# Performance work log

Hardware: AMD Instinct MI355X
Metric: run time of the kernel (lower is better)

Reference implementation:

```python
import jax, jax.numpy as jnp
import numpy as np

MSA_DIM = 256
N_HEADS = 8
HEAD_DIM = 32
INNER = N_HEADS * HEAD_DIM


def setup_inputs() -> dict:
    key = jax.random.key(0)
    ks = jax.random.split(key, 8)
    B, S, L, D = 1, 256, 256, MSA_DIM
    scale = 1.0 / np.sqrt(D)
    msa = jax.random.normal(ks[0], (B, S, L, D), dtype=jnp.float32)
    return {
        "msa": msa,
        "ln_gamma": jnp.ones((D,), jnp.float32),
        "ln_beta": jnp.zeros((D,), jnp.float32),
        "W_q": jax.random.normal(ks[1], (D, INNER), jnp.float32) * scale,
        "W_k": jax.random.normal(ks[2], (D, INNER), jnp.float32) * scale,
        "W_v": jax.random.normal(ks[3], (D, INNER), jnp.float32) * scale,
        "W_g": jax.random.normal(ks[4], (D, INNER), jnp.float32) * scale,
        "b_g": jnp.zeros((INNER,), jnp.float32),
        "W_o": jax.random.normal(ks[5], (INNER, D), jnp.float32) * (1.0 / np.sqrt(INNER)),
        "b_o": jnp.zeros((D,), jnp.float32),
    }


def _layernorm(x, gamma, beta, eps=1e-5):
    mu = jnp.mean(x, axis=-1, keepdims=True)
    var = jnp.mean(jnp.square(x - mu), axis=-1, keepdims=True)
    return (x - mu) * jax.lax.rsqrt(var + eps) * gamma + beta


def reference(msa, ln_gamma, ln_beta, W_q, W_k, W_v, W_g, b_g, W_o, b_o):
    B, S, L, D = msa.shape
    factor = 1.0 / np.sqrt(HEAD_DIM)
    x = _layernorm(msa, ln_gamma, ln_beta)  # [B,S,L,D]
    def proj(W):
        return (x @ W).reshape(B, S, L, N_HEADS, HEAD_DIM)
    Q = proj(W_q) * factor
    K = proj(W_k)
    V = proj(W_v)
    # column attention: attend over the num_seqs axis (i,j) per column c
    attn = jnp.einsum('bicnh,bjcnh->bncij', Q, K)  # [B,H,L,S,S]
    attn = jax.nn.softmax(attn, axis=-1)
    gate = jax.nn.sigmoid(x @ W_g + b_g).reshape(B, S, L, N_HEADS, HEAD_DIM)
    out = jnp.einsum('bncij,bjcnh->bicnh', attn, V) * gate
    out = out.reshape(B, S, L, INNER)
    return out @ W_o + b_o
```

## Files before the change

### kernel.cpp

```cpp
#include <hip/hip_runtime.h>
#include <hip/hip_bf16.h>


typedef __attribute__((ext_vector_type(8))) short bf16x8;
typedef __attribute__((ext_vector_type(4))) float fx4;

__device__ __forceinline__ fx4 mfma(bf16x8 a, bf16x8 b, fx4 c) {
  return __builtin_amdgcn_mfma_f32_16x16x32_bf16(a, b, c, 0, 0, 0);
}
__device__ __forceinline__ fx4 fx4zero() {
  fx4 z;
  z[0] = 0.f; z[1] = 0.f; z[2] = 0.f; z[3] = 0.f;
  return z;
}
__device__ __forceinline__ unsigned short f2bf(float f) {
  unsigned u = __float_as_uint(f);
  u += 0x7fffu + ((u >> 16) & 1u);
  return (unsigned short)(u >> 16);
}
__device__ __forceinline__ float bf2f(unsigned short h) {
  return __uint_as_float(((unsigned)h) << 16);
}
__device__ __forceinline__ unsigned pk2(float a, float b) {
  __hip_bfloat162 t = __float22bfloat162_rn(make_float2(a, b));
  return *reinterpret_cast<unsigned*>(&t);
}
__device__ __forceinline__ float asf(unsigned u) { return __uint_as_float(u); }
__device__ __forceinline__ unsigned shflu(unsigned v, int src) {
  return (unsigned)__shfl((int)v, src, 64);
}

__global__ __launch_bounds__(256) void k_wprep(
    const float* __restrict__ Wq, const float* __restrict__ Wk,
    const float* __restrict__ Wv, const float* __restrict__ Wg,
    const float* __restrict__ Wo, const float* __restrict__ gamma,
    const float* __restrict__ beta,
    unsigned short* __restrict__ wch, unsigned short* __restrict__ wcl,
    unsigned short* __restrict__ woh, unsigned short* __restrict__ wol,
    float* __restrict__ uarr, float* __restrict__ tarr) {
  __shared__ float red[8];
  const int n = blockIdx.x, k = threadIdx.x;
  const int lane = k & 63, wid = k >> 6;
  if (n < 1024) {
    int h = n >> 7, nl = n & 127, m = nl >> 5, col = h * 32 + (nl & 31);
    const float* W = (m == 0) ? Wq : (m == 1) ? Wk : (m == 2) ? Wv : Wg;
    float v = W[k * 256 + col];
    if (m == 0) v *= 0.17677669529663687f;
    float w2 = gamma[k] * v;
    unsigned short hi = f2bf(w2);
    wch[(size_t)n * 256 + k] = hi;
    wcl[(size_t)n * 256 + k] = f2bf(w2 - bf2f(hi));
    float u = w2, t = beta[k] * v;
#pragma unroll
    for (int d = 1; d < 64; d <<= 1) {
      u += __shfl_xor(u, d);
      t += __shfl_xor(t, d);
    }
    if (lane == 0) { red[wid] = u; red[4 + wid] = t; }
    __syncthreads();
    if (k == 0) {
      uarr[n] = red[0] + red[1] + red[2] + red[3];
      tarr[n] = red[4] + red[5] + red[6] + red[7];
    }
  } else {
    int nn = n - 1024;
    float v = Wo[k * 256 + nn];
    unsigned short hi = f2bf(v);
    woh[(size_t)nn * 256 + k] = hi;
    wol[(size_t)nn * 256 + k] = f2bf(v - bf2f(hi));
  }
}

__global__ __launch_bounds__(256) void k_pre(
    const float* __restrict__ msa,
    unsigned short* __restrict__ xh, unsigned short* __restrict__ xl,
    float2* __restrict__ stats) {
  int rid = blockIdx.x * 4 + (threadIdx.x >> 6);
  int lane = threadIdx.x & 63;
  float4 v = ((const float4*)(msa + (size_t)rid * 256))[lane];
  float s = v.x + v.y + v.z + v.w;
  float ss = v.x * v.x + v.y * v.y + v.z * v.z + v.w * v.w;
#pragma unroll
  for (int d = 1; d < 64; d <<= 1) {
    s += __shfl_xor(s, d);
    ss += __shfl_xor(ss, d);
  }
  unsigned h01 = pk2(v.x, v.y);
  unsigned h23 = pk2(v.z, v.w);
  float l0 = v.x - asf(h01 << 16);
  float l1 = v.y - asf(h01 & 0xffff0000u);
  float l2 = v.z - asf(h23 << 16);
  float l3 = v.w - asf(h23 & 0xffff0000u);
  uint2 hh, ll;
  hh.x = h01; hh.y = h23;
  ll.x = pk2(l0, l1); ll.y = pk2(l2, l3);
  int srow = rid >> 8, l = rid & 255;
  size_t o = ((size_t)(l * 256 + srow)) * 256 + lane * 4;
  *(uint2*)(xh + o) = hh;
  *(uint2*)(xl + o) = ll;
  if (lane == 0) {
    float mu = s * (1.f / 256.f);
    float rstd = rsqrtf(ss * (1.f / 256.f) - mu * mu + 1e-5f);
    stats[l * 256 + srow] = make_float2(mu, rstd);
  }
}

#define N_WAH 0
#define N_WAL 10240
#define N_WBH 20480
#define N_WBL 30720
#define N_KH 0
#define N_KL 20480
#define N_VTH 40960
#define N_VTL 57856

__global__ __launch_bounds__(512, 4) void k_fused_pre(
    const float* __restrict__ bg,
    const unsigned short* __restrict__ wch, const unsigned short* __restrict__ wcl,
    const float* __restrict__ uarr, const float* __restrict__ tarr,
    const unsigned short* __restrict__ xh, const unsigned short* __restrict__ xl,
    const float2* __restrict__ stats,
    float* __restrict__ O) {
  __shared__ __align__(16) char smem[74752];
  const int tid = threadIdx.x, lane = tid & 63, wid = tid >> 6;
  const int l15 = lane & 15, q4 = lane >> 4;
  const int l = (blockIdx.x & 7) * 32 + (blockIdx.x >> 6);
  const int h = (blockIdx.x >> 3) & 7;
  const size_t xbase = ((size_t)l * 256) * 256;

  fx4 acc[2][8];
#pragma unroll
  for (int i = 0; i < 2; ++i)
#pragma unroll
    for (int j = 0; j < 8; ++j) acc[i][j] = fx4zero();

  const int snl = tid >> 2, skc = tid & 3;
  const size_t wgi = (size_t)(h * 128 + snl) * 256 + skc * 8;
  const int soff = snl * 80 + skc * 16;

  {
    *(int4*)&smem[N_WAH + soff] = *(const int4*)(wch + wgi);
    *(int4*)&smem[N_WAL + soff] = *(const int4*)(wcl + wgi);
  }
  __syncthreads();

  for (int c = 0; c < 8; ++c) {
    int4 wnh, wnl;
    if (c < 7) {
      wnh = *(const int4*)(wch + wgi + (c + 1) * 32);
      wnl = *(const int4*)(wcl + wgi + (c + 1) * 32);
    }
    bf16x8 xa[2], xb[2];
#pragma unroll
    for (int fi = 0; fi < 2; ++fi) {
      size_t ga = xbase + (size_t)(wid * 32 + fi * 16 + l15) * 256 + c * 32 + q4 * 8;
      xa[fi] = *(const bf16x8*)(xh + ga);
      xb[fi] = *(const bf16x8*)(xl + ga);
    }
    const int wbh = (c & 1) ? N_WBH : N_WAH;
#pragma unroll
    for (int nh = 0; nh < 2; ++nh) {
#pragma unroll
      for (int fj = 0; fj < 4; ++fj) {
        int off = (nh * 64 + fj * 16 + l15) * 80 + q4 * 16;
        bf16x8 bh = *(const bf16x8*)&smem[wbh + off];
        bf16x8 bl = *(const bf16x8*)&smem[wbh + 10240 + off];
#pragma unroll
        for (int fi = 0; fi < 2; ++fi) {
          fx4 a = acc[fi][nh * 4 + fj];
          a = mfma(xa[fi], bh, a);
          a = mfma(xb[fi], bh, a);
          a = mfma(xa[fi], bl, a);
          acc[fi][nh * 4 + fj] = a;
        }
      }
    }
    if (c < 7) {
      const int wb2 = (c & 1) ? N_WAH : N_WBH;
      *(int4*)&smem[wb2 + soff] = wnh;
      *(int4*)&smem[wb2 + 10240 + soff] = wnl;
      __syncthreads();
    }
  }
  __syncthreads();

  float uv[8], tv[8];
#pragma unroll
  for (int fj = 0; fj < 8; ++fj) {
    int ng = h * 128 + fj * 16 + l15;
    uv[fj] = uarr[ng];
    tv[fj] = tarr[ng];
  }
  float bgv[2];
#pragma unroll
  for (int fd = 0; fd < 2; ++fd) bgv[fd] = bg[h * 32 + fd * 16 + l15];
  const int cb = l15 * 2;
  const int qbh = wid * 2560, qbl = 20480 + wid * 2560;

#pragma unroll
  for (int fi = 0; fi < 2; ++fi)
#pragma unroll
    for (int r = 0; r < 4; ++r) {
      int s = wid * 32 + fi * 16 + q4 * 4 + r;
      int il = fi * 16 + q4 * 4 + r;
      float2 st = stats[l * 256 + s];
      float y0 = st.y * (acc[fi][0][r] - st.x * uv[0]) + tv[0];
      float y1 = st.y * (acc[fi][1][r] - st.x * uv[1]) + tv[1];
      unsigned hp = pk2(y0, y1);
      unsigned lp = pk2(y0 - asf(hp << 16), y1 - asf(hp & 0xffff0000u));
      *(unsigned short*)&smem[qbh + il * 80 + cb] = (unsigned short)hp;
      *(unsigned short*)&smem[qbh + il * 80 + 32 + cb] = (unsigned short)(hp >> 16);
      *(unsigned short*)&smem[qbl + il * 80 + cb] = (unsigned short)lp;
      *(unsigned short*)&smem[qbl + il * 80 + 32 + cb] = (unsigned short)(lp >> 16);
    }
  asm volatile("s_waitcnt lgkmcnt(0)" ::: "memory");
  __builtin_amdgcn_sched_barrier(0);
  bf16x8 qh[2], ql[2];
#pragma unroll
  for (int fi = 0; fi < 2; ++fi) {
    int off = (fi * 16 + l15) * 80 + q4 * 16;
    qh[fi] = *(const bf16x8*)&smem[qbh + off];
    ql[fi] = *(const bf16x8*)&smem[qbl + off];
  }

  float gt[2][2][4];
#pragma unroll
  for (int fi = 0; fi < 2; ++fi) {
    float y4[4], y5[4];
#pragma unroll
    for (int r = 0; r < 4; ++r) {
      int s = wid * 32 + fi * 16 + q4 * 4 + r;
      float2 st = stats[l * 256 + s];
      {
        float y0 = st.y * (acc[fi][2][r] - st.x * uv[2]) + tv[2];
        float y1 = st.y * (acc[fi][3][r] - st.x * uv[3]) + tv[3];
        unsigned hp = pk2(y0, y1);
        unsigned lp = pk2(y0 - asf(hp << 16), y1 - asf(hp & 0xffff0000u));
        *(unsigned short*)&smem[N_KH + s * 80 + cb] = (unsigned short)hp;
        *(unsigned short*)&smem[N_KH + s * 80 + 32 + cb] = (unsigned short)(hp >> 16);
        *(unsigned short*)&smem[N_KL + s * 80 + cb] = (unsigned short)lp;
        *(unsigned short*)&smem[N_KL + s * 80 + 32 + cb] = (unsigned short)(lp >> 16);
      }
      y4[r] = st.y * (acc[fi][4][r] - st.x * uv[4]) + tv[4];
      y5[r] = st.y * (acc[fi][5][r] - st.x * uv[5]) + tv[5];
      float y6 = st.y * (acc[fi][6][r] - st.x * uv[6]) + tv[6];
      float y7 = st.y * (acc[fi][7][r] - st.x * uv[7]) + tv[7];
      gt[fi][0][r] = 1.f / (1.f + __expf(-(y6 + bgv[0])));
      gt[fi][1][r] = 1.f / (1.f + __expf(-(y7 + bgv[1])));
    }
    int s0 = wid * 32 + fi * 16 + q4 * 4;
    uint2 vh4, vl4, vh5, vl5;
    vh4.x = pk2(y4[0], y4[1]); vh4.y = pk2(y4[2], y4[3]);
    vl4.x = pk2(y4[0] - asf(vh4.x << 16), y4[1] - asf(vh4.x & 0xffff0000u));
    vl4.y = pk2(y4[2] - asf(vh4.y << 16), y4[3] - asf(vh4.y & 0xffff0000u));
    vh5.x = pk2(y5[0], y5[1]); vh5.y = pk2(y5[2], y5[3]);
    vl5.x = pk2(y5[0] - asf(vh5.x << 16), y5[1] - asf(vh5.x & 0xffff0000u));
    vl5.y = pk2(y5[2] - asf(vh5.y << 16), y5[3] - asf(vh5.y & 0xffff0000u));
    *(uint2*)&smem[N_VTH + l15 * 528 + s0 * 2] = vh4;
    *(uint2*)&smem[N_VTH + (16 + l15) * 528 + s0 * 2] = vh5;
    *(uint2*)&smem[N_VTL + l15 * 528 + s0 * 2] = vl4;
    *(uint2*)&smem[N_VTL + (16 + l15) * 528 + s0 * 2] = vl5;
  }
  __syncthreads();

  fx4 oacc[2][2];
  float lsum[2] = {0.f, 0.f};
  oacc[0][0] = fx4zero(); oacc[0][1] = fx4zero();
  oacc[1][0] = fx4zero(); oacc[1][1] = fx4zero();

  const int srcA = ((q4 & 1) << 5) + l15;
  const int srcB = srcA + 16;
  const bool fhi = (q4 >> 1) != 0;

  for (int jc = 0; jc < 8; ++jc) {
    const int j0 = jc * 32;
    bf16x8 kh[2], kl[2];
#pragma unroll
    for (int fj = 0; fj < 2; ++fj) {
      int off = (j0 + fj * 16 + l15) * 80 + q4 * 16;
      kh[fj] = *(const bf16x8*)&smem[N_KH + off];
      kl[fj] = *(const bf16x8*)&smem[N_KL + off];
    }
    bf16x8 vbh[2], vbl[2];
#pragma unroll
    for (int fd = 0; fd < 2; ++fd) {
      int off = (fd * 16 + l15) * 528 + j0 * 2 + q4 * 16;
      vbh[fd] = *(const bf16x8*)&smem[N_VTH + off];
      vbl[fd] = *(const bf16x8*)&smem[N_VTL + off];
    }
    fx4 sT[2][2];
    __builtin_amdgcn_s_setprio(1);
#pragma unroll
    for (int fi = 0; fi < 2; ++fi)
#pragma unroll
      for (int fj = 0; fj < 2; ++fj) {
        fx4 a = mfma(kh[fj], qh[fi], fx4zero());
        a = mfma(kh[fj], ql[fi], a);
        a = mfma(kl[fj], qh[fi], a);
        sT[fi][fj] = a;
      }
    __builtin_amdgcn_s_setprio(0);
#pragma unroll
    for (int fi = 0; fi < 2; ++fi) {
      float p0[4], p1[4];
#pragma unroll
      for (int r = 0; r < 4; ++r) {
        p0[r] = __expf(sT[fi][0][r]);
        p1[r] = __expf(sT[fi][1][r]);
      }
      lsum[fi] += ((p0[0] + p0[1]) + (p0[2] + p0[3])) +
                  ((p1[0] + p1[1]) + (p1[2] + p1[3]));
      unsigned A0 = pk2(p0[0], p0[1]), A1 = pk2(p0[2], p0[3]);
      unsigned B0 = pk2(p1[0], p1[1]), B1 = pk2(p1[2], p1[3]);
      unsigned a0A = shflu(A0, srcA), b0A = shflu(B0, srcA);
      unsigned a1A = shflu(A1, srcA), b1A = shflu(B1, srcA);
      unsigned a0B = shflu(A0, srcB), b0B = shflu(B0, srcB);
      unsigned a1B = shflu(A1, srcB), b1B = shflu(B1, srcB);
      int4 wh;
      wh.x = (int)(fhi ? b0A : a0A);
      wh.y = (int)(fhi ? b1A : a1A);
      wh.z = (int)(fhi ? b0B : a0B);
      wh.w = (int)(fhi ? b1B : a1B);
      bf16x8 pah = *reinterpret_cast<bf16x8*>(&wh);
      __builtin_amdgcn_s_setprio(1);
#pragma unroll
      for (int fd = 0; fd < 2; ++fd) {
        fx4 a = oacc[fi][fd];
        a = mfma(pah, vbh[fd], a);
        a = mfma(pah, vbl[fd], a);
        oacc[fi][fd] = a;
      }
      __builtin_amdgcn_s_setprio(0);
    }
  }

  float lsr[2][4];
#pragma unroll
  for (int fi = 0; fi < 2; ++fi) {
    float t = lsum[fi];
    t += __shfl_xor(t, 16);
    t += __shfl_xor(t, 32);
#pragma unroll
    for (int r = 0; r < 4; ++r)
      lsr[fi][r] = __shfl(t, q4 * 4 + r, 64);
  }

#pragma unroll
  for (int fi = 0; fi < 2; ++fi)
#pragma unroll
    for (int r = 0; r < 4; ++r) {
      float inv = 1.f / lsr[fi][r];
      int s = wid * 32 + fi * 16 + q4 * 4 + r;
#pragma unroll
      for (int fd = 0; fd < 2; ++fd) {
        int hd = fd * 16 + l15;
        O[((size_t)(s * 256 + l)) * 256 + h * 32 + hd] =
            oacc[fi][fd][r] * inv * gt[fi][fd][r];
      }
    }
}

#define S_XH 0
#define S_XL 20480
#define S_WH 40960
#define S_WL 51200
#define S_KPH 0
#define S_KPL 20480
#define S_VTH 40960
#define S_VTL 57856
#define S_QPH 74752
#define S_QPL 95232
#define S_ST 115712

__global__ __launch_bounds__(512, 2) void k_fused_fb(
    const float* __restrict__ msa, const float* __restrict__ bg,
    const unsigned short* __restrict__ wch, const unsigned short* __restrict__ wcl,
    const float* __restrict__ uarr, const float* __restrict__ tarr,
    float* __restrict__ O) {
  __shared__ __align__(16) char smem[117760];
  const int tid = threadIdx.x, lane = tid & 63, wid = tid >> 6;
  const int l = blockIdx.x >> 3, h = blockIdx.x & 7;

  fx4 acc[2][8];
#pragma unroll
  for (int i = 0; i < 2; ++i)
#pragma unroll
    for (int j = 0; j < 8; ++j) acc[i][j] = fx4zero();

  float st_s[4], st_ss[4];
#pragma unroll
  for (int p = 0; p < 4; ++p) { st_s[p] = 0.f; st_ss[p] = 0.f; }

  for (int c = 0; c < 8; ++c) {
    const int k0 = c * 32;
    if (c) __syncthreads();
#pragma unroll
    for (int p = 0; p < 4; ++p) {
      int srow = p * 64 + wid * 8 + (lane >> 3);
      int c4 = (lane & 7) * 4;
      float4 v = *(const float4*)(msa + ((size_t)(srow * 256 + l)) * 256 + k0 + c4);
      st_s[p] += v.x + v.y + v.z + v.w;
      st_ss[p] += v.x * v.x + v.y * v.y + v.z * v.z + v.w * v.w;
      unsigned h01 = pk2(v.x, v.y), h23 = pk2(v.z, v.w);
      float l0 = v.x - asf(h01 << 16), l1 = v.y - asf(h01 & 0xffff0000u);
      float l2 = v.z - asf(h23 << 16), l3 = v.w - asf(h23 & 0xffff0000u);
      uint2 hh, ll;
      hh.x = h01; hh.y = h23;
      ll.x = pk2(l0, l1); ll.y = pk2(l2, l3);
      *(uint2*)&smem[S_XH + srow * 80 + c4 * 2] = hh;
      *(uint2*)&smem[S_XL + srow * 80 + c4 * 2] = ll;
    }
    {
      int nl = wid * 16 + (lane >> 2);
      int kc = (lane & 3);
      size_t gi = (size_t)(h * 128 + nl) * 256 + k0 + kc * 8;
      *(int4*)&smem[S_WH + nl * 80 + kc * 16] = *(const int4*)(wch + gi);
      *(int4*)&smem[S_WL + nl * 80 + kc * 16] = *(const int4*)(wcl + gi);
    }
    __syncthreads();
    bf16x8 ah[2], al[2];
#pragma unroll
    for (int fi = 0; fi < 2; ++fi) {
      int off = (wid * 32 + fi * 16 + (lane & 15)) * 80 + (lane >> 4) * 16;
      ah[fi] = *(const bf16x8*)&smem[S_XH + off];
      al[fi] = *(const bf16x8*)&smem[S_XL + off];
    }
#pragma unroll
    for (int nh = 0; nh < 2; ++nh) {
#pragma unroll
      for (int fj = 0; fj < 4; ++fj) {
        int off = (nh * 64 + fj * 16 + (lane & 15)) * 80 + (lane >> 4) * 16;
        bf16x8 bh = *(const bf16x8*)&smem[S_WH + off];
        bf16x8 bl = *(const bf16x8*)&smem[S_WL + off];
#pragma unroll
        for (int fi = 0; fi < 2; ++fi) {
          fx4 a = acc[fi][nh * 4 + fj];
          a = mfma(ah[fi], bh, a);
          a = mfma(al[fi], bh, a);
          a = mfma(ah[fi], bl, a);
          acc[fi][nh * 4 + fj] = a;
        }
      }
    }
  }

#pragma unroll
  for (int p = 0; p < 4; ++p) {
    float s_ = st_s[p], ss_ = st_ss[p];
    s_ += __shfl_xor(s_, 1); ss_ += __shfl_xor(ss_, 1);
    s_ += __shfl_xor(s_, 2); ss_ += __shfl_xor(ss_, 2);
    s_ += __shfl_xor(s_, 4); ss_ += __shfl_xor(ss_, 4);
    if ((lane & 7) == 0) {
      int row = p * 64 + wid * 8 + (lane >> 3);
      float mu = s_ * (1.f / 256.f);
      float rstd = rsqrtf(ss_ * (1.f / 256.f) - mu * mu + 1e-5f);
      *(float2*)&smem[S_ST + row * 8] = make_float2(mu, rstd);
    }
  }
  __syncthreads();

  float uv[8], tv[8];
#pragma unroll
  for (int fj = 0; fj < 8; ++fj) {
    int ng = h * 128 + fj * 16 + (lane & 15);
    uv[fj] = uarr[ng];
    tv[fj] = tarr[ng];
  }
  float bgv[2];
#pragma unroll
  for (int fd = 0; fd < 2; ++fd) bgv[fd] = bg[h * 32 + fd * 16 + (lane & 15)];
  float gt[2][2][4];
#pragma unroll
  for (int fi = 0; fi < 2; ++fi)
#pragma unroll
    for (int r = 0; r < 4; ++r) {
      int s = wid * 32 + fi * 16 + (lane >> 4) * 4 + r;
      float2 st = *(const float2*)&smem[S_ST + s * 8];
#pragma unroll
      for (int fj = 0; fj < 8; ++fj) {
        int col = fj * 16 + (lane & 15);
        float y = st.y * (acc[fi][fj][r] - st.x * uv[fj]) + tv[fj];
        unsigned short hv = f2bf(y);
        unsigned short lv = f2bf(y - bf2f(hv));
        if (fj < 2) {
          *(unsigned short*)&smem[S_QPH + s * 80 + col * 2] = hv;
          *(unsigned short*)&smem[S_QPL + s * 80 + col * 2] = lv;
        } else if (fj < 4) {
          *(unsigned short*)&smem[S_KPH + s * 80 + (col - 32) * 2] = hv;
          *(unsigned short*)&smem[S_KPL + s * 80 + (col - 32) * 2] = lv;
        } else if (fj < 6) {
          *(unsigned short*)&smem[S_VTH + (col - 64) * 528 + s * 2] = hv;
          *(unsigned short*)&smem[S_VTL + (col - 64) * 528 + s * 2] = lv;
        } else {
          gt[fi][fj - 6][r] = 1.f / (1.f + __expf(-(y + bgv[fj - 6])));
        }
      }
    }
  __syncthreads();

  const int i0 = wid * 32;
  bf16x8 qh[2], ql[2];
#pragma unroll
  for (int fi = 0; fi < 2; ++fi) {
    int off = (i0 + fi * 16 + (lane & 15)) * 80 + (lane >> 4) * 16;
    qh[fi] = *(const bf16x8*)&smem[S_QPH + off];
    ql[fi] = *(const bf16x8*)&smem[S_QPL + off];
  }

  fx4 oacc[2][2];
  float lrun[2][4];
#pragma unroll
  for (int a = 0; a < 2; ++a) {
    oacc[a][0] = fx4zero();
    oacc[a][1] = fx4zero();
#pragma unroll
    for (int r = 0; r < 4; ++r) lrun[a][r] = 0.f;
  }

  for (int jc = 0; jc < 8; ++jc) {
    const int j0 = jc * 32;
    bf16x8 kh[2], kl[2];
#pragma unroll
    for (int fj = 0; fj < 2; ++fj) {
      int off = (j0 + fj * 16 + (lane & 15)) * 80 + (lane >> 4) * 16;
      kh[fj] = *(const bf16x8*)&smem[S_KPH + off];
      kl[fj] = *(const bf16x8*)&smem[S_KPL + off];
    }
    bf16x8 vbh[2], vbl[2];
#pragma unroll
    for (int fd = 0; fd < 2; ++fd) {
      int off = (fd * 16 + (lane & 15)) * 528 + j0 * 2 + (lane >> 4) * 16;
      vbh[fd] = *(const bf16x8*)&smem[S_VTH + off];
      vbl[fd] = *(const bf16x8*)&smem[S_VTL + off];
    }
    fx4 sacc[2][2];
#pragma unroll
    for (int fi = 0; fi < 2; ++fi)
#pragma unroll
      for (int fj = 0; fj < 2; ++fj) {
        fx4 a = mfma(qh[fi], kh[fj], fx4zero());
        a = mfma(qh[fi], kl[fj], a);
        a = mfma(ql[fi], kh[fj], a);
        sacc[fi][fj] = a;
      }
#pragma unroll
    for (int fi = 0; fi < 2; ++fi)
#pragma unroll
      for (int r = 0; r < 4; ++r) {
        float p0 = __expf(sacc[fi][0][r]);
        float p1 = __expf(sacc[fi][1][r]);
        lrun[fi][r] += p0 + p1;
        int il = fi * 16 + (lane >> 4) * 4 + r;
        unsigned short h0 = f2bf(p0), h1 = f2bf(p1);
        unsigned short s0 = f2bf(p0 - bf2f(h0)), s1 = f2bf(p1 - bf2f(h1));
        *(unsigned short*)&smem[S_QPH + wid * 2560 + il * 80 + (lane & 15) * 2] = h0;
        *(unsigned short*)&smem[S_QPH + wid * 2560 + il * 80 + 32 + (lane & 15) * 2] = h1;
        *(unsigned short*)&smem[S_QPL + wid * 2560 + il * 80 + (lane & 15) * 2] = s0;
        *(unsigned short*)&smem[S_QPL + wid * 2560 + il * 80 + 32 + (lane & 15) * 2] = s1;
      }
    asm volatile("s_waitcnt lgkmcnt(0)" ::: "memory");
    __builtin_amdgcn_sched_barrier(0);
    bf16x8 pah[2], pal[2];
#pragma unroll
    for (int fi = 0; fi < 2; ++fi) {
      int off = wid * 2560 + (fi * 16 + (lane & 15)) * 80 + (lane >> 4) * 16;
      pah[fi] = *(const bf16x8*)&smem[S_QPH + off];
      pal[fi] = *(const bf16x8*)&smem[S_QPL + off];
    }
#pragma unroll
    for (int fi = 0; fi < 2; ++fi)
#pragma unroll
      for (int fd = 0; fd < 2; ++fd) {
        fx4 a = oacc[fi][fd];
        a = mfma(pah[fi], vbh[fd], a);
        a = mfma(pal[fi], vbh[fd], a);
        a = mfma(pah[fi], vbl[fd], a);
        oacc[fi][fd] = a;
      }
  }

#pragma unroll
  for (int fi = 0; fi < 2; ++fi)
#pragma unroll
    for (int r = 0; r < 4; ++r) {
      float t = lrun[fi][r];
      t += __shfl_xor(t, 1);
      t += __shfl_xor(t, 2);
      t += __shfl_xor(t, 4);
      t += __shfl_xor(t, 8);
      lrun[fi][r] = t;
    }

#pragma unroll
  for (int fi = 0; fi < 2; ++fi)
#pragma unroll
    for (int fd = 0; fd < 2; ++fd)
#pragma unroll
      for (int r = 0; r < 4; ++r) {
        int s = i0 + fi * 16 + (lane >> 4) * 4 + r;
        int hd = fd * 16 + (lane & 15);
        float ov = oacc[fi][fd][r] / lrun[fi][r];
        O[((size_t)(s * 256 + l)) * 256 + h * 32 + hd] = ov * gt[fi][fd][r];
      }
}

__global__ __launch_bounds__(256, 2) void k_final(
    float* __restrict__ O, const unsigned short* __restrict__ woh,
    const unsigned short* __restrict__ wol, const float* __restrict__ bo) {
  __shared__ __align__(16) char smem[51200];
  const int tid = threadIdx.x, lane = tid & 63, wid = tid >> 6;
  const int m0 = blockIdx.x * 64;
  fx4 acc[4][4];
#pragma unroll
  for (int i = 0; i < 4; ++i)
#pragma unroll
    for (int j = 0; j < 4; ++j) acc[i][j] = fx4zero();

  for (int c = 0; c < 8; ++c) {
    const int k0 = c * 32;
    if (c) __syncthreads();
#pragma unroll
    for (int p = 0; p < 2; ++p) {
      int row = p * 32 + wid * 8 + (lane >> 3);
      int c4 = (lane & 7) * 4;
      float4 v = *(const float4*)(O + (size_t)(m0 + row) * 256 + k0 + c4);
      unsigned h01 = pk2(v.x, v.y), h23 = pk2(v.z, v.w);
      float l0 = v.x - asf(h01 << 16), l1 = v.y - asf(h01 & 0xffff0000u);
      float l2 = v.z - asf(h23 << 16), l3 = v.w - asf(h23 & 0xffff0000u);
      uint2 hh, ll;
      hh.x = h01; hh.y = h23;
      ll.x = pk2(l0, l1); ll.y = pk2(l2, l3);
      *(uint2*)&smem[0 + row * 80 + c4 * 2] = hh;
      *(uint2*)&smem[5120 + row * 80 + c4 * 2] = ll;
    }
#pragma unroll
    for (int p = 0; p < 4; ++p) {
      int nl = p * 64 + wid * 16 + (lane >> 2);
      int kc = (lane & 3);
      size_t gi = (size_t)nl * 256 + k0 + kc * 8;
      *(int4*)&smem[10240 + nl * 80 + kc * 16] = *(const int4*)(woh + gi);
      *(int4*)&smem[30720 + nl * 80 + kc * 16] = *(const int4*)(wol + gi);
    }
    __syncthreads();
    bf16x8 ah[4], al[4];
#pragma unroll
    for (int fi = 0; fi < 4; ++fi) {
      int off = (fi * 16 + (lane & 15)) * 80 + (lane >> 4) * 16;
      ah[fi] = *(const bf16x8*)&smem[0 + off];
      al[fi] = *(const bf16x8*)&smem[5120 + off];
    }
#pragma unroll
    for (int fj = 0; fj < 4; ++fj) {
      int off = (wid * 64 + fj * 16 + (lane & 15)) * 80 + (lane >> 4) * 16;
      bf16x8 bh = *(const bf16x8*)&smem[10240 + off];
      bf16x8 bl = *(const bf16x8*)&smem[30720 + off];
#pragma unroll
      for (int fi = 0; fi < 4; ++fi) {
        fx4 a = acc[fi][fj];
        a = mfma(ah[fi], bh, a);
        a = mfma(al[fi], bh, a);
        a = mfma(ah[fi], bl, a);
        acc[fi][fj] = a;
      }
    }
  }
#pragma unroll
  for (int fi = 0; fi < 4; ++fi)
#pragma unroll
    for (int fj = 0; fj < 4; ++fj)
#pragma unroll
      for (int r = 0; r < 4; ++r) {
        int m = m0 + fi * 16 + (lane >> 4) * 4 + r;
        int n = wid * 64 + fj * 16 + (lane & 15);
        O[(size_t)m * 256 + n] = acc[fi][fj][r] + bo[n];
      }
}

extern "C" void kernel_launch(void* const* d_in, const int* in_sizes, int n_in,
                              void* d_out, int out_size, void* d_ws, size_t ws_size,
                              hipStream_t stream) {
  const float* msa   = (const float*)d_in[0];
  const float* gamma = (const float*)d_in[1];
  const float* beta  = (const float*)d_in[2];
  const float* Wq    = (const float*)d_in[3];
  const float* Wk    = (const float*)d_in[4];
  const float* Wv    = (const float*)d_in[5];
  const float* Wg    = (const float*)d_in[6];
  const float* bg    = (const float*)d_in[7];
  const float* Wo    = (const float*)d_in[8];
  const float* bo    = (const float*)d_in[9];

  char* ws = (char*)d_ws;
  unsigned short* wch = (unsigned short*)(ws);
  unsigned short* wcl = (unsigned short*)(ws + 524288);
  unsigned short* woh = (unsigned short*)(ws + 1048576);
  unsigned short* wol = (unsigned short*)(ws + 1179648);
  float* uarr = (float*)(ws + 1310720);
  float* tarr = (float*)(ws + 1314816);

  const size_t XOFF = 2097152ull;
  unsigned short* xh = (unsigned short*)(ws + XOFF);
  unsigned short* xl = (unsigned short*)(ws + XOFF + 33554432ull);
  float2* stats = (float2*)(ws + XOFF + 67108864ull);
  const bool pre = ws_size >= XOFF + 67108864ull + 524288ull;

  float* out = (float*)d_out;

  k_wprep<<<1280, 256, 0, stream>>>(Wq, Wk, Wv, Wg, Wo, gamma, beta,
                                    wch, wcl, woh, wol, uarr, tarr);
  if (pre) {
    k_pre<<<16384, 256, 0, stream>>>(msa, xh, xl, stats);
    k_fused_pre<<<2048, 512, 0, stream>>>(bg, wch, wcl, uarr, tarr,
                                          xh, xl, stats, out);
  } else {
    k_fused_fb<<<2048, 512, 0, stream>>>(msa, bg, wch, wcl, uarr, tarr, out);
  }
  k_final<<<1024, 256, 0, stream>>>(out, woh, wol, bo);
}
```

Measured before the change: 226.3 us.

## Stage weight tiles in two large halves instead of eight double-buffered chunks

The projection GEMM used to stream the weight slice through shared memory in eight 32-wide K chunks, double-buffered with a barrier after each chunk. It now loads half of K (128 columns) at once into a larger padded shared buffer, with one barrier per half, and runs four unrolled K steps from it. This removes most of the per-chunk barriers and lets all loads for a half be in flight together. In exchange it drops the overlap between the next chunk's prefetch and the current chunk's MFMAs, and puts more data in shared memory, though it still fits the existing 74752-byte array.

Result: faster. 212.3 us (-6.2%).

```diff
diff --git a/kernel.cpp b/kernel.cpp
--- a/kernel.cpp
+++ b/kernel.cpp
@@ -105,10 +105,8 @@
   }
 }
 
-#define N_WAH 0
-#define N_WAL 10240
-#define N_WBH 20480
-#define N_WBL 30720
+#define N_W0H 0
+#define N_W0L 34816
 #define N_KH 0
 #define N_KL 20480
 #define N_VTH 40960
@@ -134,52 +132,44 @@
 #pragma unroll
     for (int j = 0; j < 8; ++j) acc[i][j] = fx4zero();
 
-  const int snl = tid >> 2, skc = tid & 3;
-  const size_t wgi = (size_t)(h * 128 + snl) * 256 + skc * 8;
-  const int soff = snl * 80 + skc * 16;
-
-  {
-    *(int4*)&smem[N_WAH + soff] = *(const int4*)(wch + wgi);
-    *(int4*)&smem[N_WAL + soff] = *(const int4*)(wcl + wgi);
-  }
-  __syncthreads();
-
-  for (int c = 0; c < 8; ++c) {
-    int4 wnh, wnl;
-    if (c < 7) {
-      wnh = *(const int4*)(wch + wgi + (c + 1) * 32);
-      wnl = *(const int4*)(wcl + wgi + (c + 1) * 32);
-    }
-    bf16x8 xa[2], xb[2];
-#pragma unroll
-    for (int fi = 0; fi < 2; ++fi) {
-      size_t ga = xbase + (size_t)(wid * 32 + fi * 16 + l15) * 256 + c * 32 + q4 * 8;
-      xa[fi] = *(const bf16x8*)(xh + ga);
-      xb[fi] = *(const bf16x8*)(xl + ga);
-    }
-    const int wbh = (c & 1) ? N_WBH : N_WAH;
-#pragma unroll
-    for (int nh = 0; nh < 2; ++nh) {
-#pragma unroll
-      for (int fj = 0; fj < 4; ++fj) {
-        int off = (nh * 64 + fj * 16 + l15) * 80 + q4 * 16;
-        bf16x8 bh = *(const bf16x8*)&smem[wbh + off];
-        bf16x8 bl = *(const bf16x8*)&smem[wbh + 10240 + off];
-#pragma unroll
-        for (int fi = 0; fi < 2; ++fi) {
-          fx4 a = acc[fi][nh * 4 + fj];
-          a = mfma(xa[fi], bh, a);
-          a = mfma(xb[fi], bh, a);
-          a = mfma(xa[fi], bl, a);
-          acc[fi][nh * 4 + fj] = a;
+  for (int hf = 0; hf < 2; ++hf) {
+    if (hf) __syncthreads();
+#pragma unroll
+    for (int p = 0; p < 4; ++p) {
+      int id = p * 512 + tid;
+      int nl = id >> 4, qc = id & 15;
+      size_t g = (size_t)(h * 128 + nl) * 256 + hf * 128 + qc * 8;
+      *(int4*)&smem[N_W0H + nl * 272 + qc * 16] = *(const int4*)(wch + g);
+      *(int4*)&smem[N_W0L + nl * 272 + qc * 16] = *(const int4*)(wcl + g);
+    }
+    __syncthreads();
+#pragma unroll
+    for (int cc = 0; cc < 4; ++cc) {
+      const int c = hf * 4 + cc;
+      bf16x8 xa[2], xb[2];
+#pragma unroll
+      for (int fi = 0; fi < 2; ++fi) {
+        size_t ga = xbase + (size_t)(wid * 32 + fi * 16 + l15) * 256 + c * 32 + q4 * 8;
+        xa[fi] = *(const bf16x8*)(xh + ga);
+        xb[fi] = *(const bf16x8*)(xl + ga);
+      }
+#pragma unroll
+      for (int nh = 0; nh < 2; ++nh) {
+#pragma unroll
+        for (int fj = 0; fj < 4; ++fj) {
+          int off = (nh * 64 + fj * 16 + l15) * 272 + cc * 64 + q4 * 16;
+          bf16x8 bh = *(const bf16x8*)&smem[N_W0H + off];
+          bf16x8 bl = *(const bf16x8*)&smem[N_W0L + off];
+#pragma unroll
+          for (int fi = 0; fi < 2; ++fi) {
+            fx4 a = acc[fi][nh * 4 + fj];
+            a = mfma(xa[fi], bh, a);
+            a = mfma(xb[fi], bh, a);
+            a = mfma(xa[fi], bl, a);
+            acc[fi][nh * 4 + fj] = a;
+          }
         }
       }
-    }
-    if (c < 7) {
-      const int wb2 = (c & 1) ? N_WAH : N_WBH;
-      *(int4*)&smem[wb2 + soff] = wnh;
-      *(int4*)&smem[wb2 + 10240 + soff] = wnl;
-      __syncthreads();
     }
   }
   __syncthreads();
```
